# Kernel tuning notes

Measured on AMD Instinct MI355X. Metric: run time of the kernel, lower is better.

The kernel has to match this reference:

```python
import jax, jax.numpy as jnp
import numpy as np

N_HEAD = 12


def setup_inputs() -> dict:
    key = jax.random.key(0)
    ks = jax.random.split(key, 16)
    B, N, D, P, H = 1, 512, 384, 128, N_HEAD
    s = 0.02
    return {
        'x1d': jax.random.normal(ks[0], (B, N, D), jnp.float32),
        'x2d': jax.random.normal(ks[1], (B, N, N, P), jnp.float32),
        'pose_t': jax.random.normal(ks[2], (B, N, 3), jnp.float32),
        'pose_r': jax.random.normal(ks[3], (B, N, 3, 3), jnp.float32),
        'bias': jnp.zeros((B, 1, N, N), jnp.float32),
        'w_sq': jax.random.normal(ks[4], (D, D), jnp.float32) * s,
        'w_sk': jax.random.normal(ks[5], (D, D), jnp.float32) * s,
        'w_sv': jax.random.normal(ks[6], (D, D), jnp.float32) * s,
        'w_pb': jax.random.normal(ks[7], (P, H), jnp.float32) * s,
        'w_pq': jax.random.normal(ks[8], (D, H * 3 * 4), jnp.float32) * s,
        'w_pk': jax.random.normal(ks[9], (D, H * 3 * 4), jnp.float32) * s,
        'w_pv': jax.random.normal(ks[10], (D, H * 3 * 8), jnp.float32) * s,
        'tpw': jax.random.uniform(ks[11], (H,), jnp.float32),
        'w_pairv': jax.random.normal(ks[12], (P, D), jnp.float32) * s,
        'w_out': jax.random.normal(ks[13], (2 * D + H * 8 * 4, D), jnp.float32) * s,
        'b_out': jnp.zeros((D,), jnp.float32),
    }


def reference(x1d, x2d, pose_t, pose_r, bias, w_sq, w_sk, w_sv, w_pb,
              w_pq, w_pk, w_pv, tpw, w_pairv, w_out, b_out):
    B, N, D = x1d.shape
    H = N_HEAD
    dk = D // H
    scalar_w = 1.0 / np.sqrt(3 * dk)
    point_w_c = 1.0 / np.sqrt(3 * 4 * 9 / 2)
    pair_w = 1.0 / np.sqrt(3)

    T = pose_t                                # [B,N,3]
    R = jnp.swapaxes(pose_r, -1, -2)          # [B,N,3,3] (pose[1]^T as in torch code)

    # scalar attention
    q_s = (x1d @ w_sq).reshape(B, N, H, dk)
    k_s = (x1d @ w_sk).reshape(B, N, H, dk)
    v_s = (x1d @ w_sv).reshape(B, N, H, dk)
    scalar_attn = jnp.einsum('bihc,bjhc->bhij', q_s * scalar_w, k_s)

    # point attention (global frame)
    def affine(pt):  # R @ pt + T
        return jnp.einsum('bnxy,bnhpy->bnhpx', R, pt) + T[:, :, None, None, :]

    q_p = affine((x1d @ w_pq).reshape(B, N, H, 4, 3))
    k_p = affine((x1d @ w_pk).reshape(B, N, H, 4, 3))
    v_p = affine((x1d @ w_pv).reshape(B, N, H, 8, 3))

    dist = jnp.linalg.norm(q_p[:, :, None] - k_p[:, None], axis=-1)  # [B,I,J,H,P]
    pw = point_w_c * jax.nn.softplus(tpw)                            # [H]
    point_attn = -0.5 * pw[:, None, None] * jnp.transpose(dist.sum(-1), (0, 3, 1, 2))

    # pair bias attention
    pair_attn = pair_w * jnp.transpose(x2d @ w_pb, (0, 3, 1, 2))     # [B,H,I,J]

    attn = jax.nn.softmax(scalar_attn + point_attn + pair_attn + bias, axis=-1)

    # aggregations
    out_scalar = jnp.einsum('bhij,bjhc->bihc', attn, v_s).reshape(B, N, D)

    out_pg = jnp.einsum('bhij,bjhcp->bihcp', attn, v_p)              # [B,I,H,8,3]
    # inverse affine: R^T @ (x - T)
    out_pl = jnp.einsum('bnyx,bnhpy->bnhpx', R, out_pg - T[:, :, None, None, :])
    out_pn = jnp.linalg.norm(out_pl, axis=-1).reshape(B, N, H * 8)
    out_pl = out_pl.reshape(B, N, H * 8 * 3)

    v_pair = (x2d @ w_pairv).reshape(B, N, N, H, dk)
    out_pair = jnp.einsum('bhij,bijhc->bihc', attn, v_pair).reshape(B, N, D)

    feat = jnp.concatenate([out_scalar, out_pl, out_pair, out_pn], axis=-1)
    return feat @ w_out + b_out
```

## Files before the change

### kernel.cpp

```cpp
#include <hip/hip_runtime.h>
#include <hip/hip_bf16.h>
#include <math.h>

#define N_  512
#define D_  384
#define H_  12
#define DK_ 32
#define P_  128

typedef short short8 __attribute__((ext_vector_type(8)));
typedef float f32x4  __attribute__((ext_vector_type(4)));

static __device__ __forceinline__ unsigned short f2bf(float f) {
    union { float f; unsigned int u; } v; v.f = f;
    unsigned int r = (v.u + 0x7FFFu + ((v.u >> 16) & 1u)) >> 16;
    return (unsigned short)r;
}

static __device__ __forceinline__ short2 pk2bf(float a, float b) {
    __hip_bfloat162 h = __float22bfloat162_rn(make_float2(a, b));
    return *(short2*)&h;
}

typedef union { short8 v; short2 h2[4]; } s8u;

__global__ __launch_bounds__(384) void k_proj(
    const float* __restrict__ x1d, const float* __restrict__ pose_t,
    const float* __restrict__ pose_r,
    const float* __restrict__ w_sq, const float* __restrict__ w_sk,
    const float* __restrict__ w_sv, const float* __restrict__ w_pq,
    const float* __restrict__ w_pk, const float* __restrict__ w_pv,
    float* __restrict__ qs, float* __restrict__ kst,
    float* __restrict__ qp, float* __restrict__ kpt,
    unsigned short* __restrict__ vcatT)
{
    const int seg = blockIdx.y;
    const int i0  = blockIdx.x * 8;
    const int t   = threadIdx.x;

    __shared__ float raw[8][288];
    __shared__ float Rsh[8][9];
    __shared__ float Tsh[8][3];

    if (seg < 3) {
        const float* __restrict__ w = (seg == 0) ? w_sq : (seg == 1) ? w_sk : w_sv;
        float acc[8];
        #pragma unroll
        for (int r = 0; r < 8; ++r) acc[r] = 0.f;
        for (int d = 0; d < D_; d += 4) {
            float4 xr[8];
            #pragma unroll
            for (int r = 0; r < 8; ++r)
                xr[r] = *(const float4*)(x1d + (i0 + r) * D_ + d);
            #pragma unroll
            for (int e = 0; e < 4; ++e) {
                float wv = w[(d + e) * D_ + t];
                #pragma unroll
                for (int r = 0; r < 8; ++r)
                    acc[r] += ((const float*)&xr[r])[e] * wv;
            }
        }
        if (seg == 0) {
            #pragma unroll
            for (int r = 0; r < 8; ++r) qs[(i0 + r) * D_ + t] = acc[r];
        } else if (seg == 1) {
            *(float4*)(kst + t * N_ + i0)     = make_float4(acc[0], acc[1], acc[2], acc[3]);
            *(float4*)(kst + t * N_ + i0 + 4) = make_float4(acc[4], acc[5], acc[6], acc[7]);
        } else {
            int h = t >> 5, c = t & 31;
            s8u sv;
            #pragma unroll
            for (int r = 0; r < 4; ++r) sv.h2[r] = pk2bf(acc[2*r], acc[2*r+1]);
            *(short8*)(vcatT + ((size_t)h * 64 + c) * N_ + i0) = sv.v;
        }
    } else {
        if (t < 72) Rsh[t / 9][t % 9] = pose_r[(i0 + t / 9) * 9 + t % 9];
        else if (t < 96) {
            int r = (t - 72) / 3, c = (t - 72) % 3;
            Tsh[r][c] = pose_t[(i0 + r) * 3 + c];
        }

        if (t < 288) {
            const float* __restrict__ w;
            int col, ldw;
            if (seg == 3) {
                if (t < 144) { w = w_pq; col = t;       ldw = 144; }
                else         { w = w_pk; col = t - 144; ldw = 144; }
            } else         { w = w_pv; col = t;       ldw = 288; }
            float acc[8];
            #pragma unroll
            for (int r = 0; r < 8; ++r) acc[r] = 0.f;
            for (int d = 0; d < D_; d += 4) {
                float4 xr[8];
                #pragma unroll
                for (int r = 0; r < 8; ++r)
                    xr[r] = *(const float4*)(x1d + (i0 + r) * D_ + d);
                #pragma unroll
                for (int e = 0; e < 4; ++e) {
                    float wv = w[(d + e) * ldw + col];
                    #pragma unroll
                    for (int r = 0; r < 8; ++r)
                        acc[r] += ((const float*)&xr[r])[e] * wv;
                }
            }
            #pragma unroll
            for (int r = 0; r < 8; ++r) raw[r][t] = acc[r];
        }
        __syncthreads();

        if (t < 288) {
            const int x3   = t % 3;
            const int base = t - x3;
            if (seg == 3) {
                const int c = (t < 144) ? t : t - 144;
                if (t < 144) {
                    #pragma unroll
                    for (int r = 0; r < 8; ++r) {
                        float g = Rsh[r][0 + x3] * raw[r][base]
                                + Rsh[r][3 + x3] * raw[r][base + 1]
                                + Rsh[r][6 + x3] * raw[r][base + 2] + Tsh[r][x3];
                        qp[(i0 + r) * 144 + c] = g;
                    }
                } else {
                    float g[8];
                    #pragma unroll
                    for (int r = 0; r < 8; ++r)
                        g[r] = Rsh[r][0 + x3] * raw[r][base]
                             + Rsh[r][3 + x3] * raw[r][base + 1]
                             + Rsh[r][6 + x3] * raw[r][base + 2] + Tsh[r][x3];
                    *(float4*)(kpt + c * N_ + i0)     = make_float4(g[0], g[1], g[2], g[3]);
                    *(float4*)(kpt + c * N_ + i0 + 4) = make_float4(g[4], g[5], g[6], g[7]);
                }
            } else {
                int h = t / 24, pc = t % 24;
                float g[8];
                #pragma unroll
                for (int r = 0; r < 8; ++r)
                    g[r] = Rsh[r][0 + x3] * raw[r][base]
                         + Rsh[r][3 + x3] * raw[r][base + 1]
                         + Rsh[r][6 + x3] * raw[r][base + 2] + Tsh[r][x3];
                s8u sv;
                #pragma unroll
                for (int r = 0; r < 4; ++r) sv.h2[r] = pk2bf(g[2*r], g[2*r+1]);
                *(short8*)(vcatT + ((size_t)h * 64 + 32 + pc) * N_ + i0) = sv.v;
            }
        }
    }
}

__global__ __launch_bounds__(256) void k_logits_pair(
    const float* __restrict__ x2d, const float* __restrict__ w_pb,
    float* __restrict__ logits)
{
    const int t    = threadIdx.x;
    const int wid  = t >> 6;
    const int lane = t & 63;
    const int quad = lane >> 4;
    const int col  = lane & 15;
    const float pair_w = 0.57735027f;

    short8 bfr[4];
    #pragma unroll
    for (int kt = 0; kt < 4; ++kt) {
        #pragma unroll
        for (int jj = 0; jj < 8; ++jj) {
            int p = kt * 32 + quad * 8 + jj;
            bfr[kt][jj] = (col < 12) ? (short)f2bf(w_pb[p * 12 + col]) : (short)0;
        }
    }

    #pragma unroll
    for (int s = 0; s < 2; ++s) {
        const int T  = blockIdx.x * 8 + wid * 2 + s;
        const int i  = T >> 5;
        const int j0 = (T & 31) << 4;
        const float* xrow = x2d + ((size_t)(i * N_) + j0 + col) * P_;

        f32x4 acc = {0.f, 0.f, 0.f, 0.f};
        #pragma unroll
        for (int kt = 0; kt < 4; ++kt) {
            const int k0 = kt * 32 + quad * 8;
            float4 f0 = *(const float4*)(xrow + k0);
            float4 f1 = *(const float4*)(xrow + k0 + 4);
            s8u afr;
            afr.h2[0] = pk2bf(f0.x, f0.y);
            afr.h2[1] = pk2bf(f0.z, f0.w);
            afr.h2[2] = pk2bf(f1.x, f1.y);
            afr.h2[3] = pk2bf(f1.z, f1.w);
            acc = __builtin_amdgcn_mfma_f32_16x16x32_bf16(afr.v, bfr[kt], acc, 0, 0, 0);
        }
        if (col < 12) {
            #pragma unroll
            for (int r = 0; r < 4; ++r) {
                int j = j0 + quad * 4 + r;
                logits[((size_t)(col * N_ + i)) * N_ + j] = pair_w * acc[r];
            }
        }
    }
}

__global__ __launch_bounds__(256) void k_logits_sp(
    const float* __restrict__ qs, const float* __restrict__ kst,
    const float* __restrict__ qp, const float* __restrict__ kpt,
    const float* __restrict__ bias, const float* __restrict__ tpw,
    float* __restrict__ logits)
{
    const int h  = blockIdx.x / 128;
    const int i0 = (blockIdx.x % 128) * 4;
    const int t  = threadIdx.x;
    __shared__ float qsh[4][32];
    __shared__ float qph[4][12];
    if (t < 128) { int il = t / 32, c = t % 32; qsh[il][c] = qs[(i0+il) * D_ + h*32 + c]; }
    else if (t < 176) { int r = t - 128; int il = r / 12, c = r % 12; qph[il][c] = qp[(i0+il)*144 + h*12 + c]; }
    const float pwh = 0.13608276f * log1pf(expf(tpw[h]));
    const float scalar_w = 0.10206207f;
    __syncthreads();

    for (int jh = 0; jh < 2; ++jh) {
        int j = t + jh * 256;
        float kv[32];
        #pragma unroll
        for (int c = 0; c < 32; ++c) kv[c] = kst[(h*32 + c) * N_ + j];
        float kp[12];
        #pragma unroll
        for (int c = 0; c < 12; ++c) kp[c] = kpt[(h*12 + c) * N_ + j];

        #pragma unroll
        for (int il = 0; il < 4; ++il) {
            float s = 0.f;
            #pragma unroll
            for (int c = 0; c < 32; ++c) s += qsh[il][c] * kv[c];
            float dsum = 0.f;
            #pragma unroll
            for (int p = 0; p < 4; ++p) {
                float dx = qph[il][p*3+0] - kp[p*3+0];
                float dy = qph[il][p*3+1] - kp[p*3+1];
                float dz = qph[il][p*3+2] - kp[p*3+2];
                dsum += sqrtf(dx*dx + dy*dy + dz*dz);
            }
            size_t idx = ((size_t)(h * N_ + (i0+il))) * N_ + j;
            logits[idx] += scalar_w * s - 0.5f * pwh * dsum + bias[(i0+il) * N_ + j];
        }
    }
}

__global__ __launch_bounds__(256) void k_softmax(float* __restrict__ logits,
                                                 unsigned short* __restrict__ attn_bf)
{
    const int row = blockIdx.x;
    const int t = threadIdx.x;
    float* ptr = logits + (size_t)row * N_;
    __shared__ float red[256];

    float a = ptr[t], b = ptr[t + 256];
    red[t] = fmaxf(a, b);
    __syncthreads();
    for (int s = 128; s > 0; s >>= 1) {
        if (t < s) red[t] = fmaxf(red[t], red[t + s]);
        __syncthreads();
    }
    float m = red[0];
    __syncthreads();
    float ea = __expf(a - m), eb = __expf(b - m);
    red[t] = ea + eb;
    __syncthreads();
    for (int s = 128; s > 0; s >>= 1) {
        if (t < s) red[t] += red[t + s];
        __syncthreads();
    }
    float inv = 1.0f / red[0];
    float pa = ea * inv, pb = eb * inv;
    ptr[t]       = pa;
    ptr[t + 256] = pb;
    attn_bf[(size_t)row * N_ + t]       = f2bf(pa);
    attn_bf[(size_t)row * N_ + t + 256] = f2bf(pb);
}

__global__ __launch_bounds__(256) void k_tmp(
    const float* __restrict__ attn, const float* __restrict__ x2d,
    float* __restrict__ tmp)
{
    const int i = blockIdx.x;
    const int t = threadIdx.x;
    __shared__ float4 at[3][N_];
    __shared__ float red[4][1536];

    for (int idx = t; idx < 12 * 128; idx += 256) {
        int h = idx >> 7, j4 = (idx & 127) << 2;
        float4 a = *(const float4*)(attn + ((size_t)(h * N_ + i)) * N_ + j4);
        int g = h >> 2, c = h & 3;
        ((float*)&at[g][j4 + 0])[c] = a.x;
        ((float*)&at[g][j4 + 1])[c] = a.y;
        ((float*)&at[g][j4 + 2])[c] = a.z;
        ((float*)&at[g][j4 + 3])[c] = a.w;
    }
    __syncthreads();

    const int p2 = (t & 63) * 2;
    const int jh = t >> 6;
    float acc[12][2];
    #pragma unroll
    for (int h = 0; h < 12; ++h) { acc[h][0] = 0.f; acc[h][1] = 0.f; }
    const float* xb = x2d + (size_t)i * N_ * P_;

    #pragma unroll 4
    for (int j = jh; j < N_; j += 4) {
        float2 x = *(const float2*)(xb + j * P_ + p2);
        float4 a0 = at[0][j], a1 = at[1][j], a2 = at[2][j];
        acc[0][0]  += a0.x*x.x; acc[0][1]  += a0.x*x.y;
        acc[1][0]  += a0.y*x.x; acc[1][1]  += a0.y*x.y;
        acc[2][0]  += a0.z*x.x; acc[2][1]  += a0.z*x.y;
        acc[3][0]  += a0.w*x.x; acc[3][1]  += a0.w*x.y;
        acc[4][0]  += a1.x*x.x; acc[4][1]  += a1.x*x.y;
        acc[5][0]  += a1.y*x.x; acc[5][1]  += a1.y*x.y;
        acc[6][0]  += a1.z*x.x; acc[6][1]  += a1.z*x.y;
        acc[7][0]  += a1.w*x.x; acc[7][1]  += a1.w*x.y;
        acc[8][0]  += a2.x*x.x; acc[8][1]  += a2.x*x.y;
        acc[9][0]  += a2.y*x.x; acc[9][1]  += a2.y*x.y;
        acc[10][0] += a2.z*x.x; acc[10][1] += a2.z*x.y;
        acc[11][0] += a2.w*x.x; acc[11][1] += a2.w*x.y;
    }
    #pragma unroll
    for (int h = 0; h < 12; ++h) {
        red[jh][h * 128 + p2]     = acc[h][0];
        red[jh][h * 128 + p2 + 1] = acc[h][1];
    }
    __syncthreads();
    for (int idx = t; idx < 1536; idx += 256)
        tmp[(size_t)i * 1536 + idx] = red[0][idx] + red[1][idx] + red[2][idx] + red[3][idx];
}

__global__ __launch_bounds__(256) void k_aggr(
    const unsigned short* __restrict__ attn_bf,
    const unsigned short* __restrict__ vcatT,
    float* __restrict__ feat, float* __restrict__ outpg)
{
    const int h  = blockIdx.x >> 5;
    const int i0 = (blockIdx.x & 31) << 4;
    const int t    = threadIdx.x;
    const int wid  = t >> 6;
    const int lane = t & 63;
    const int quad = lane >> 4;
    const int col  = lane & 15;
    const int c    = wid * 16 + col;
    const bool cvalid = (c < 56);

    const unsigned short* arow = attn_bf + ((size_t)(h * N_ + i0 + col)) * N_;
    const unsigned short* brow = vcatT + ((size_t)h * 64 + c) * N_;

    f32x4 acc = {0.f, 0.f, 0.f, 0.f};
    #pragma unroll
    for (int kt = 0; kt < 16; ++kt) {
        const int k0 = kt * 32 + quad * 8;
        short8 a = *(const short8*)(arow + k0);
        short8 b;
        if (cvalid) b = *(const short8*)(brow + k0);
        else { b[0]=0;b[1]=0;b[2]=0;b[3]=0;b[4]=0;b[5]=0;b[6]=0;b[7]=0; }
        acc = __builtin_amdgcn_mfma_f32_16x16x32_bf16(a, b, acc, 0, 0, 0);
    }
    #pragma unroll
    for (int r = 0; r < 4; ++r) {
        int i = i0 + quad * 4 + r;
        if (c < 32)       feat[(size_t)i * 1152 + h * 32 + c] = acc[r];
        else if (c < 56)  outpg[((size_t)i * 12 + h) * 24 + (c - 32)] = acc[r];
    }
}

__global__ __launch_bounds__(384) void k_feat(
    const float* __restrict__ tmp, const float* __restrict__ outpg,
    const float* __restrict__ pose_t, const float* __restrict__ pose_r,
    const float* __restrict__ w_pairv, float* __restrict__ feat)
{
    const int i = blockIdx.x;
    const int t = threadIdx.x;
    __shared__ float tsh[1536];
    __shared__ float pg[288];
    __shared__ float pl[288];
    __shared__ float Rsh[9], Tsh[3];

    for (int idx = t; idx < 1536; idx += 384) tsh[idx] = tmp[(size_t)i * 1536 + idx];
    if (t < 288) pg[t] = outpg[i * 288 + t];
    if (t < 9) Rsh[t] = pose_r[i * 9 + t];
    if (t < 3) Tsh[t] = pose_t[i * 3 + t];
    __syncthreads();

    {
        int h = t >> 5;
        const float* ts = tsh + h * 128;
        float acc = 0.f;
        #pragma unroll 4
        for (int p = 0; p < 128; ++p) acc += ts[p] * w_pairv[p * D_ + t];
        feat[(size_t)i * 1152 + 672 + t] = acc;
    }
    if (t < 288) {
        int x3 = t % 3, base = t - x3;
        float g0 = pg[base + 0] - Tsh[0];
        float g1 = pg[base + 1] - Tsh[1];
        float g2 = pg[base + 2] - Tsh[2];
        float v = Rsh[x3*3+0]*g0 + Rsh[x3*3+1]*g1 + Rsh[x3*3+2]*g2;
        pl[t] = v;
        feat[(size_t)i * 1152 + 384 + t] = v;
    }
    __syncthreads();
    if (t < 96) {
        float a = pl[t*3], b = pl[t*3+1], c = pl[t*3+2];
        feat[(size_t)i * 1152 + 1056 + t] = sqrtf(a*a + b*b + c*c);
    }
}

__global__ __launch_bounds__(384) void k_out_part(
    const float* __restrict__ feat, const float* __restrict__ w_out,
    float* __restrict__ part)
{
    const int kc = blockIdx.x >> 6;
    const int i0 = (blockIdx.x & 63) * 8;
    const int t  = threadIdx.x;
    const int k0 = kc * 144;

    float acc[8];
    #pragma unroll
    for (int r = 0; r < 8; ++r) acc[r] = 0.f;

    for (int d = 0; d < 144; d += 4) {
        float4 fr[8];
        #pragma unroll
        for (int r = 0; r < 8; ++r)
            fr[r] = *(const float4*)(feat + (size_t)(i0 + r) * 1152 + k0 + d);
        #pragma unroll
        for (int e = 0; e < 4; ++e) {
            float wv = w_out[(size_t)(k0 + d + e) * D_ + t];
            #pragma unroll
            for (int r = 0; r < 8; ++r)
                acc[r] += ((const float*)&fr[r])[e] * wv;
        }
    }
    #pragma unroll
    for (int r = 0; r < 8; ++r)
        part[((size_t)kc * N_ + i0 + r) * D_ + t] = acc[r];
}

__global__ __launch_bounds__(256) void k_out_red(
    const float* __restrict__ part, const float* __restrict__ b_out,
    float* __restrict__ out)
{
    const int idx = blockIdx.x * 256 + threadIdx.x;
    float s = b_out[idx % D_];
    #pragma unroll
    for (int kc = 0; kc < 8; ++kc) s += part[(size_t)kc * (N_ * D_) + idx];
    out[idx] = s;
}

extern "C" void kernel_launch(void* const* d_in, const int* in_sizes, int n_in,
                              void* d_out, int out_size, void* d_ws, size_t ws_size,
                              hipStream_t stream)
{
    (void)in_sizes; (void)n_in; (void)out_size; (void)ws_size;
    const float* x1d     = (const float*)d_in[0];
    const float* x2d     = (const float*)d_in[1];
    const float* pose_t  = (const float*)d_in[2];
    const float* pose_r  = (const float*)d_in[3];
    const float* bias    = (const float*)d_in[4];
    const float* w_sq    = (const float*)d_in[5];
    const float* w_sk    = (const float*)d_in[6];
    const float* w_sv    = (const float*)d_in[7];
    const float* w_pb    = (const float*)d_in[8];
    const float* w_pq    = (const float*)d_in[9];
    const float* w_pk    = (const float*)d_in[10];
    const float* w_pv    = (const float*)d_in[11];
    const float* tpw     = (const float*)d_in[12];
    const float* w_pairv = (const float*)d_in[13];
    const float* w_out   = (const float*)d_in[14];
    const float* b_out   = (const float*)d_in[15];
    float* out = (float*)d_out;

    float* ws = (float*)d_ws;
    float* qs     = ws;
    float* kst    = qs     + 196608;
    float* qp     = kst    + 196608;
    float* kpt    = qp     + 73728;
    float* logits = kpt    + 73728;
    float* tmp    = logits + 3145728;
    float* outpg  = tmp    + 786432;
    float* feat   = outpg  + 147456;
    float* part   = feat   + 589824;
    unsigned short* attn_bf = (unsigned short*)(part + 1572864);
    unsigned short* vcatT   = attn_bf + (size_t)12 * N_ * N_;

    hipLaunchKernelGGL(k_logits_pair, dim3(2048), dim3(256), 0, stream,
                       x2d, w_pb, logits);
    hipLaunchKernelGGL(k_proj, dim3(64, 5), dim3(384), 0, stream,
                       x1d, pose_t, pose_r, w_sq, w_sk, w_sv, w_pq, w_pk, w_pv,
                       qs, kst, qp, kpt, vcatT);
    hipLaunchKernelGGL(k_logits_sp, dim3(12 * 128), dim3(256), 0, stream,
                       qs, kst, qp, kpt, bias, tpw, logits);
    hipLaunchKernelGGL(k_softmax, dim3(12 * N_), dim3(256), 0, stream,
                       logits, attn_bf);
    hipLaunchKernelGGL(k_tmp, dim3(N_), dim3(256), 0, stream,
                       logits, x2d, tmp);
    hipLaunchKernelGGL(k_aggr, dim3(12 * 32), dim3(256), 0, stream,
                       attn_bf, vcatT, feat, outpg);
    hipLaunchKernelGGL(k_feat, dim3(N_), dim3(384), 0, stream,
                       tmp, outpg, pose_t, pose_r, w_pairv, feat);
    hipLaunchKernelGGL(k_out_part, dim3(512), dim3(384), 0, stream,
                       feat, w_out, part);
    hipLaunchKernelGGL(k_out_red, dim3(768), dim3(256), 0, stream,
                       part, b_out, out);
}
```

Before: 392.3 us.

## Fuse pair-logit and projection kernels, fold softmax into logits, merge mid stages

```diff
diff --git a/kernel.cpp b/kernel.cpp
--- a/kernel.cpp
+++ b/kernel.cpp
@@ -16,15 +16,19 @@
     unsigned int r = (v.u + 0x7FFFu + ((v.u >> 16) & 1u)) >> 16;
     return (unsigned short)r;
 }
-
+static __device__ __forceinline__ float bf2f(unsigned short u) {
+    union { unsigned int u; float f; } v; v.u = ((unsigned int)u) << 16;
+    return v.f;
+}
 static __device__ __forceinline__ short2 pk2bf(float a, float b) {
     __hip_bfloat162 h = __float22bfloat162_rn(make_float2(a, b));
     return *(short2*)&h;
 }
-
 typedef union { short8 v; short2 h2[4]; } s8u;
 
-__global__ __launch_bounds__(384) void k_proj(
+__global__ __launch_bounds__(384) void k_front(
+    const float* __restrict__ x2d, const float* __restrict__ w_pb,
+    float* __restrict__ pairlog,
     const float* __restrict__ x1d, const float* __restrict__ pose_t,
     const float* __restrict__ pose_r,
     const float* __restrict__ w_sq, const float* __restrict__ w_sk,
@@ -34,13 +38,63 @@
     float* __restrict__ qp, float* __restrict__ kpt,
     unsigned short* __restrict__ vcatT)
 {
-    const int seg = blockIdx.y;
-    const int i0  = blockIdx.x * 8;
-    const int t   = threadIdx.x;
-
     __shared__ float raw[8][288];
     __shared__ float Rsh[8][9];
     __shared__ float Tsh[8][3];
+
+    const int t = threadIdx.x;
+
+    if (blockIdx.x < 2048) {
+        if (t >= 256) return;
+        const int wid  = t >> 6;
+        const int lane = t & 63;
+        const int quad = lane >> 4;
+        const int col  = lane & 15;
+        const float pair_w = 0.57735027f;
+
+        short8 bfr[4];
+        #pragma unroll
+        for (int kt = 0; kt < 4; ++kt) {
+            #pragma unroll
+            for (int jj = 0; jj < 8; ++jj) {
+                int p = kt * 32 + quad * 8 + jj;
+                bfr[kt][jj] = (col < 12) ? (short)f2bf(w_pb[p * 12 + col]) : (short)0;
+            }
+        }
+        #pragma unroll
+        for (int s = 0; s < 2; ++s) {
+            const int T  = blockIdx.x * 8 + wid * 2 + s;
+            const int i  = T >> 5;
+            const int j0 = (T & 31) << 4;
+            const float* xrow = x2d + ((size_t)(i * N_) + j0 + col) * P_;
+
+            f32x4 acc = {0.f, 0.f, 0.f, 0.f};
+            #pragma unroll
+            for (int kt = 0; kt < 4; ++kt) {
+                const int k0 = kt * 32 + quad * 8;
+                float4 f0 = *(const float4*)(xrow + k0);
+                float4 f1 = *(const float4*)(xrow + k0 + 4);
+                s8u afr;
+                afr.h2[0] = pk2bf(f0.x, f0.y);
+                afr.h2[1] = pk2bf(f0.z, f0.w);
+                afr.h2[2] = pk2bf(f1.x, f1.y);
+                afr.h2[3] = pk2bf(f1.z, f1.w);
+                acc = __builtin_amdgcn_mfma_f32_16x16x32_bf16(afr.v, bfr[kt], acc, 0, 0, 0);
+            }
+            if (col < 12) {
+                #pragma unroll
+                for (int r = 0; r < 4; ++r) {
+                    int j = j0 + quad * 4 + r;
+                    pairlog[((size_t)(col * N_ + i)) * N_ + j] = pair_w * acc[r];
+                }
+            }
+        }
+        return;
+    }
+
+    const int b   = blockIdx.x - 2048;
+    const int seg = b >> 6;
+    const int i0  = (b & 63) * 8;
 
     if (seg < 3) {
         const float* __restrict__ w = (seg == 0) ? w_sq : (seg == 1) ? w_sk : w_sv;
@@ -148,74 +202,29 @@
     }
 }
 
-__global__ __launch_bounds__(256) void k_logits_pair(
-    const float* __restrict__ x2d, const float* __restrict__ w_pb,
-    float* __restrict__ logits)
-{
-    const int t    = threadIdx.x;
-    const int wid  = t >> 6;
-    const int lane = t & 63;
-    const int quad = lane >> 4;
-    const int col  = lane & 15;
-    const float pair_w = 0.57735027f;
-
-    short8 bfr[4];
-    #pragma unroll
-    for (int kt = 0; kt < 4; ++kt) {
-        #pragma unroll
-        for (int jj = 0; jj < 8; ++jj) {
-            int p = kt * 32 + quad * 8 + jj;
-            bfr[kt][jj] = (col < 12) ? (short)f2bf(w_pb[p * 12 + col]) : (short)0;
-        }
-    }
-
-    #pragma unroll
-    for (int s = 0; s < 2; ++s) {
-        const int T  = blockIdx.x * 8 + wid * 2 + s;
-        const int i  = T >> 5;
-        const int j0 = (T & 31) << 4;
-        const float* xrow = x2d + ((size_t)(i * N_) + j0 + col) * P_;
-
-        f32x4 acc = {0.f, 0.f, 0.f, 0.f};
-        #pragma unroll
-        for (int kt = 0; kt < 4; ++kt) {
-            const int k0 = kt * 32 + quad * 8;
-            float4 f0 = *(const float4*)(xrow + k0);
-            float4 f1 = *(const float4*)(xrow + k0 + 4);
-            s8u afr;
-            afr.h2[0] = pk2bf(f0.x, f0.y);
-            afr.h2[1] = pk2bf(f0.z, f0.w);
-            afr.h2[2] = pk2bf(f1.x, f1.y);
-            afr.h2[3] = pk2bf(f1.z, f1.w);
-            acc = __builtin_amdgcn_mfma_f32_16x16x32_bf16(afr.v, bfr[kt], acc, 0, 0, 0);
-        }
-        if (col < 12) {
-            #pragma unroll
-            for (int r = 0; r < 4; ++r) {
-                int j = j0 + quad * 4 + r;
-                logits[((size_t)(col * N_ + i)) * N_ + j] = pair_w * acc[r];
-            }
-        }
-    }
-}
-
-__global__ __launch_bounds__(256) void k_logits_sp(
+__global__ __launch_bounds__(256) void k_sp_soft(
     const float* __restrict__ qs, const float* __restrict__ kst,
     const float* __restrict__ qp, const float* __restrict__ kpt,
     const float* __restrict__ bias, const float* __restrict__ tpw,
-    float* __restrict__ logits)
+    const float* __restrict__ pairlog,
+    unsigned short* __restrict__ attn_bf)
 {
     const int h  = blockIdx.x / 128;
     const int i0 = (blockIdx.x % 128) * 4;
     const int t  = threadIdx.x;
+    const int lane = t & 63;
+    const int wid  = t >> 6;
     __shared__ float qsh[4][32];
     __shared__ float qph[4][12];
+    __shared__ float wredm[4][4];
+    __shared__ float wreds[4][4];
     if (t < 128) { int il = t / 32, c = t % 32; qsh[il][c] = qs[(i0+il) * D_ + h*32 + c]; }
     else if (t < 176) { int r = t - 128; int il = r / 12, c = r % 12; qph[il][c] = qp[(i0+il)*144 + h*12 + c]; }
     const float pwh = 0.13608276f * log1pf(expf(tpw[h]));
     const float scalar_w = 0.10206207f;
     __syncthreads();
 
+    float v[4][2];
     for (int jh = 0; jh < 2; ++jh) {
         int j = t + jh * 256;
         float kv[32];
@@ -238,106 +247,107 @@
                 float dz = qph[il][p*3+2] - kp[p*3+2];
                 dsum += sqrtf(dx*dx + dy*dy + dz*dz);
             }
-            size_t idx = ((size_t)(h * N_ + (i0+il))) * N_ + j;
-            logits[idx] += scalar_w * s - 0.5f * pwh * dsum + bias[(i0+il) * N_ + j];
-        }
-    }
-}
-
-__global__ __launch_bounds__(256) void k_softmax(float* __restrict__ logits,
-                                                 unsigned short* __restrict__ attn_bf)
-{
-    const int row = blockIdx.x;
-    const int t = threadIdx.x;
-    float* ptr = logits + (size_t)row * N_;
-    __shared__ float red[256];
-
-    float a = ptr[t], b = ptr[t + 256];
-    red[t] = fmaxf(a, b);
+            v[il][jh] = scalar_w * s - 0.5f * pwh * dsum
+                      + bias[(i0+il) * N_ + j]
+                      + pairlog[((size_t)(h * N_ + (i0+il))) * N_ + j];
+        }
+    }
+
+    #pragma unroll
+    for (int il = 0; il < 4; ++il) {
+        float mt = fmaxf(v[il][0], v[il][1]);
+        #pragma unroll
+        for (int off = 1; off < 64; off <<= 1)
+            mt = fmaxf(mt, __shfl_xor(mt, off));
+        if (lane == 0) wredm[il][wid] = mt;
+    }
     __syncthreads();
-    for (int s = 128; s > 0; s >>= 1) {
-        if (t < s) red[t] = fmaxf(red[t], red[t + s]);
-        __syncthreads();
-    }
-    float m = red[0];
+    float m[4];
+    #pragma unroll
+    for (int il = 0; il < 4; ++il)
+        m[il] = fmaxf(fmaxf(wredm[il][0], wredm[il][1]),
+                      fmaxf(wredm[il][2], wredm[il][3]));
+
+    #pragma unroll
+    for (int il = 0; il < 4; ++il) {
+        float e0 = __expf(v[il][0] - m[il]);
+        float e1 = __expf(v[il][1] - m[il]);
+        v[il][0] = e0; v[il][1] = e1;
+        float st = e0 + e1;
+        #pragma unroll
+        for (int off = 1; off < 64; off <<= 1)
+            st += __shfl_xor(st, off);
+        if (lane == 0) wreds[il][wid] = st;
+    }
     __syncthreads();
-    float ea = __expf(a - m), eb = __expf(b - m);
-    red[t] = ea + eb;
-    __syncthreads();
-    for (int s = 128; s > 0; s >>= 1) {
-        if (t < s) red[t] += red[t + s];
-        __syncthreads();
-    }
-    float inv = 1.0f / red[0];
-    float pa = ea * inv, pb = eb * inv;
-    ptr[t]       = pa;
-    ptr[t + 256] = pb;
-    attn_bf[(size_t)row * N_ + t]       = f2bf(pa);
-    attn_bf[(size_t)row * N_ + t + 256] = f2bf(pb);
-}
-
-__global__ __launch_bounds__(256) void k_tmp(
-    const float* __restrict__ attn, const float* __restrict__ x2d,
-    float* __restrict__ tmp)
-{
-    const int i = blockIdx.x;
-    const int t = threadIdx.x;
+    #pragma unroll
+    for (int il = 0; il < 4; ++il) {
+        float inv = 1.0f / (wreds[il][0] + wreds[il][1] + wreds[il][2] + wreds[il][3]);
+        size_t base = ((size_t)(h * N_ + i0 + il)) * N_;
+        attn_bf[base + t]       = f2bf(v[il][0] * inv);
+        attn_bf[base + t + 256] = f2bf(v[il][1] * inv);
+    }
+}
+
+__global__ __launch_bounds__(256) void k_mid(
+    const unsigned short* __restrict__ attn_bf,
+    const float* __restrict__ x2d,
+    const unsigned short* __restrict__ vcatT,
+    float* __restrict__ tmp,
+    float* __restrict__ feat, float* __restrict__ outpg)
+{
     __shared__ float4 at[3][N_];
     __shared__ float red[4][1536];
 
-    for (int idx = t; idx < 12 * 128; idx += 256) {
-        int h = idx >> 7, j4 = (idx & 127) << 2;
-        float4 a = *(const float4*)(attn + ((size_t)(h * N_ + i)) * N_ + j4);
-        int g = h >> 2, c = h & 3;
-        ((float*)&at[g][j4 + 0])[c] = a.x;
-        ((float*)&at[g][j4 + 1])[c] = a.y;
-        ((float*)&at[g][j4 + 2])[c] = a.z;
-        ((float*)&at[g][j4 + 3])[c] = a.w;
-    }
-    __syncthreads();
-
-    const int p2 = (t & 63) * 2;
-    const int jh = t >> 6;
-    float acc[12][2];
-    #pragma unroll
-    for (int h = 0; h < 12; ++h) { acc[h][0] = 0.f; acc[h][1] = 0.f; }
-    const float* xb = x2d + (size_t)i * N_ * P_;
-
-    #pragma unroll 4
-    for (int j = jh; j < N_; j += 4) {
-        float2 x = *(const float2*)(xb + j * P_ + p2);
-        float4 a0 = at[0][j], a1 = at[1][j], a2 = at[2][j];
-        acc[0][0]  += a0.x*x.x; acc[0][1]  += a0.x*x.y;
-        acc[1][0]  += a0.y*x.x; acc[1][1]  += a0.y*x.y;
-        acc[2][0]  += a0.z*x.x; acc[2][1]  += a0.z*x.y;
-        acc[3][0]  += a0.w*x.x; acc[3][1]  += a0.w*x.y;
-        acc[4][0]  += a1.x*x.x; acc[4][1]  += a1.x*x.y;
-        acc[5][0]  += a1.y*x.x; acc[5][1]  += a1.y*x.y;
-        acc[6][0]  += a1.z*x.x; acc[6][1]  += a1.z*x.y;
-        acc[7][0]  += a1.w*x.x; acc[7][1]  += a1.w*x.y;
-        acc[8][0]  += a2.x*x.x; acc[8][1]  += a2.x*x.y;
-        acc[9][0]  += a2.y*x.x; acc[9][1]  += a2.y*x.y;
-        acc[10][0] += a2.z*x.x; acc[10][1] += a2.z*x.y;
-        acc[11][0] += a2.w*x.x; acc[11][1] += a2.w*x.y;
-    }
-    #pragma unroll
-    for (int h = 0; h < 12; ++h) {
-        red[jh][h * 128 + p2]     = acc[h][0];
-        red[jh][h * 128 + p2 + 1] = acc[h][1];
-    }
-    __syncthreads();
-    for (int idx = t; idx < 1536; idx += 256)
-        tmp[(size_t)i * 1536 + idx] = red[0][idx] + red[1][idx] + red[2][idx] + red[3][idx];
-}
-
-__global__ __launch_bounds__(256) void k_aggr(
-    const unsigned short* __restrict__ attn_bf,
-    const unsigned short* __restrict__ vcatT,
-    float* __restrict__ feat, float* __restrict__ outpg)
-{
-    const int h  = blockIdx.x >> 5;
-    const int i0 = (blockIdx.x & 31) << 4;
-    const int t    = threadIdx.x;
+    const int t = threadIdx.x;
+
+    if (blockIdx.x < 512) {
+        const int i = blockIdx.x;
+        for (int idx = t; idx < 12 * N_; idx += 256) {
+            int h = idx >> 9, j = idx & 511;
+            float a = bf2f(attn_bf[((size_t)(h * N_ + i)) * N_ + j]);
+            ((float*)&at[h >> 2][j])[h & 3] = a;
+        }
+        __syncthreads();
+
+        const int p2 = (t & 63) * 2;
+        const int jh = t >> 6;
+        float acc[12][2];
+        #pragma unroll
+        for (int h = 0; h < 12; ++h) { acc[h][0] = 0.f; acc[h][1] = 0.f; }
+        const float* xb = x2d + (size_t)i * N_ * P_;
+
+        #pragma unroll 4
+        for (int j = jh; j < N_; j += 4) {
+            float2 x = *(const float2*)(xb + j * P_ + p2);
+            float4 a0 = at[0][j], a1 = at[1][j], a2 = at[2][j];
+            acc[0][0]  += a0.x*x.x; acc[0][1]  += a0.x*x.y;
+            acc[1][0]  += a0.y*x.x; acc[1][1]  += a0.y*x.y;
+            acc[2][0]  += a0.z*x.x; acc[2][1]  += a0.z*x.y;
+            acc[3][0]  += a0.w*x.x; acc[3][1]  += a0.w*x.y;
+            acc[4][0]  += a1.x*x.x; acc[4][1]  += a1.x*x.y;
+            acc[5][0]  += a1.y*x.x; acc[5][1]  += a1.y*x.y;
+            acc[6][0]  += a1.z*x.x; acc[6][1]  += a1.z*x.y;
+            acc[7][0]  += a1.w*x.x; acc[7][1]  += a1.w*x.y;
+            acc[8][0]  += a2.x*x.x; acc[8][1]  += a2.x*x.y;
+            acc[9][0]  += a2.y*x.x; acc[9][1]  += a2.y*x.y;
+            acc[10][0] += a2.z*x.x; acc[10][1] += a2.z*x.y;
+            acc[11][0] += a2.w*x.x; acc[11][1] += a2.w*x.y;
+        }
+        #pragma unroll
+        for (int h = 0; h < 12; ++h) {
+            red[jh][h * 128 + p2]     = acc[h][0];
+            red[jh][h * 128 + p2 + 1] = acc[h][1];
+        }
+        __syncthreads();
+        for (int idx = t; idx < 1536; idx += 256)
+            tmp[(size_t)i * 1536 + idx] = red[0][idx] + red[1][idx] + red[2][idx] + red[3][idx];
+        return;
+    }
+
+    const int bid  = blockIdx.x - 512;
+    const int h    = bid >> 5;
+    const int i0   = (bid & 31) << 4;
     const int wid  = t >> 6;
     const int lane = t & 63;
     const int quad = lane >> 4;
@@ -474,31 +484,26 @@
     float* out = (float*)d_out;
 
     float* ws = (float*)d_ws;
-    float* qs     = ws;
-    float* kst    = qs     + 196608;
-    float* qp     = kst    + 196608;
-    float* kpt    = qp     + 73728;
-    float* logits = kpt    + 73728;
-    float* tmp    = logits + 3145728;
-    float* outpg  = tmp    + 786432;
-    float* feat   = outpg  + 147456;
-    float* part   = feat   + 589824;
+    float* qs      = ws;
+    float* kst     = qs      + 196608;
+    float* qp      = kst     + 196608;
+    float* kpt     = qp      + 73728;
+    float* pairlog = kpt     + 73728;
+    float* tmp     = pairlog + 3145728;
+    float* outpg   = tmp     + 786432;
+    float* feat    = outpg   + 147456;
+    float* part    = feat    + 589824;
     unsigned short* attn_bf = (unsigned short*)(part + 1572864);
     unsigned short* vcatT   = attn_bf + (size_t)12 * N_ * N_;
 
-    hipLaunchKernelGGL(k_logits_pair, dim3(2048), dim3(256), 0, stream,
-                       x2d, w_pb, logits);
-    hipLaunchKernelGGL(k_proj, dim3(64, 5), dim3(384), 0, stream,
+    hipLaunchKernelGGL(k_front, dim3(2048 + 320), dim3(384), 0, stream,
+                       x2d, w_pb, pairlog,
                        x1d, pose_t, pose_r, w_sq, w_sk, w_sv, w_pq, w_pk, w_pv,
                        qs, kst, qp, kpt, vcatT);
-    hipLaunchKernelGGL(k_logits_sp, dim3(12 * 128), dim3(256), 0, stream,
-                       qs, kst, qp, kpt, bias, tpw, logits);
-    hipLaunchKernelGGL(k_softmax, dim3(12 * N_), dim3(256), 0, stream,
-                       logits, attn_bf);
-    hipLaunchKernelGGL(k_tmp, dim3(N_), dim3(256), 0, stream,
-                       logits, x2d, tmp);
-    hipLaunchKernelGGL(k_aggr, dim3(12 * 32), dim3(256), 0, stream,
-                       attn_bf, vcatT, feat, outpg);
+    hipLaunchKernelGGL(k_sp_soft, dim3(12 * 128), dim3(256), 0, stream,
+                       qs, kst, qp, kpt, bias, tpw, pairlog, attn_bf);
+    hipLaunchKernelGGL(k_mid, dim3(512 + 384), dim3(256), 0, stream,
+                       attn_bf, x2d, vcatT, tmp, feat, outpg);
     hipLaunchKernelGGL(k_feat, dim3(N_), dim3(384), 0, stream,
                        tmp, outpg, pose_t, pose_r, w_pairv, feat);
     hipLaunchKernelGGL(k_out_part, dim3(512), dim3(384), 0, stream,
```

After: 358.9 us. 1.09x faster.
